# Optimization experiments

Hardware: AMD Instinct MI355X
Metric: run time of the kernel (lower is better)

The kernel has to match this reference:

```python
import jax, jax.numpy as jnp
import numpy as np

B, W, L = 64, 128, 32   # sentences, words per sentence, max chars per word
V, E, H = 128, 128, 256 # char vocab, char_embedding_size, word_embedding_size


def setup_inputs() -> dict:
    key = jax.random.key(0)
    ks = jax.random.split(key, 14)
    char_ids = jax.random.randint(ks[0], (B, W, L), 0, V, dtype=jnp.int32)
    word_lens = jax.random.randint(ks[1], (B, W), 1, L + 1, dtype=jnp.int32)
    sc = 1.0 / np.sqrt(H)
    n = lambda k, shape, s: (jax.random.normal(k, shape, jnp.float32) * s)
    emb_table = n(ks[2], (V, E), 1.0).at[0].set(0.0)  # padding_idx=0 row is zero
    return {
        "char_ids": char_ids,
        "word_lens": word_lens,
        "emb_table": emb_table,
        "Wih_f": n(ks[3], (4 * H, E), sc), "Whh_f": n(ks[4], (4 * H, H), sc),
        "bih_f": n(ks[5], (4 * H,), sc), "bhh_f": n(ks[6], (4 * H,), sc),
        "Wih_b": n(ks[7], (4 * H, E), sc), "Whh_b": n(ks[8], (4 * H, H), sc),
        "bih_b": n(ks[9], (4 * H,), sc), "bhh_b": n(ks[10], (4 * H,), sc),
        "pW": n(ks[11], (H, 2 * H), 1.0 / np.sqrt(2 * H)),
        "pb": n(ks[12], (H,), 1.0 / np.sqrt(2 * H)),
    }


def _lstm_dir(xW, mask, Whh, reverse):
    # xW: [N, L, 4H] precomputed x@Wih^T + biases; mask: [N, L] bool (t < len).
    # Masked scan: h/c freeze outside valid region, so the final carry is
    # h at t=len-1 (forward) or h at t=0 (backward, reverse=True).
    N = xW.shape[0]
    h0 = jnp.zeros((N, H), xW.dtype)
    c0 = jnp.zeros((N, H), xW.dtype)

    def step(carry, inp):
        h, c = carry
        xw_t, m_t = inp
        g = xw_t + h @ Whh.T                      # [N, 4H]
        i, f, gg, o = jnp.split(g, 4, axis=-1)    # PyTorch gate order i,f,g,o
        c_new = jax.nn.sigmoid(f) * c + jax.nn.sigmoid(i) * jnp.tanh(gg)
        h_new = jax.nn.sigmoid(o) * jnp.tanh(c_new)
        m = m_t[:, None]
        return (jnp.where(m, h_new, h), jnp.where(m, c_new, c)), None

    (h, _), _ = jax.lax.scan(step, (h0, c0),
                             (xW.transpose(1, 0, 2), mask.T), reverse=reverse)
    return h


def reference(char_ids, word_lens, emb_table, Wih_f, Whh_f, bih_f, bhh_f,
              Wih_b, Whh_b, bih_b, bhh_b, pW, pb):
    ids = char_ids.reshape(-1, L)                 # [N, L], N = B*W
    lens = word_lens.reshape(-1)                  # [N]
    x = emb_table[ids]                            # [N, L, E]
    mask = jnp.arange(L)[None, :] < lens[:, None] # [N, L]
    xWf = jnp.einsum('nle,ge->nlg', x, Wih_f) + (bih_f + bhh_f)
    xWb = jnp.einsum('nle,ge->nlg', x, Wih_b) + (bih_b + bhh_b)
    h_fwd = _lstm_dir(xWf, mask, Whh_f, reverse=False)  # fwd dir at last char
    h_bwd = _lstm_dir(xWb, mask, Whh_b, reverse=True)   # bwd dir at first char
    # Original concatenates (backward_at_first, forward_at_last)
    concat = jnp.concatenate([h_bwd, h_fwd], axis=-1)   # [N, 2H]
    wemb = concat @ pW.T + pb                           # [N, H]
    out = wemb.reshape(B, W, H)
    lens_out = jnp.full((B,), W, dtype=jnp.int32)       # words per sentence
    return out, lens_out
```

## Files before the change

### kernel.cpp

```cpp
#include <hip/hip_runtime.h>
#include <hip/hip_bf16.h>
#include <hip/hip_fp8.h>
#include <math.h>

#define B_  64
#define W_  128
#define L_  32
#define V_  128
#define E_  128
#define H_  256
#define G4_ 1024
#define NW  8192
#define KS_ 8
#define ROWB 264
#define HROW 264
#define M_  32

typedef long i64;
typedef short s8v  __attribute__((ext_vector_type(8)));
typedef float f4v  __attribute__((ext_vector_type(4)));

static __device__ __forceinline__ float b2f(unsigned short u) {
  return __uint_as_float(((unsigned int)u) << 16);
}
static __device__ __forceinline__ unsigned char f2fp8(float f) {
  __hip_fp8_e4m3 t(f);
  return (unsigned char)t.__x;
}
static __device__ __forceinline__ float sigm(float x) {
  return __builtin_amdgcn_rcpf(1.f + __expf(-x));
}
static __device__ __forceinline__ float tanh_(float x) {
  return __builtin_amdgcn_rcpf(1.f + __expf(-2.f * x)) * 2.f - 1.f;
}

__global__ __launch_bounds__(256) void k_embproj(
    const float* __restrict__ emb,
    const float* __restrict__ Wih_f, const float* __restrict__ bih_f, const float* __restrict__ bhh_f,
    const float* __restrict__ Wih_b, const float* __restrict__ bih_b, const float* __restrict__ bhh_b,
    unsigned short* __restrict__ ep4) {
  int v   = blockIdx.x & (V_ - 1);
  int dir = blockIdx.x >> 7;
  const float* Wih = dir ? Wih_b : Wih_f;
  const float* b1  = dir ? bih_b : bih_f;
  const float* b2  = dir ? bhh_b : bhh_f;
  __shared__ float es[E_];
  if (threadIdx.x < E_) es[threadIdx.x] = emb[v * E_ + threadIdx.x];
  __syncthreads();
#pragma unroll
  for (int q = 0; q < 4; ++q) {
    int g = q * 256 + threadIdx.x;
    const float* wr = Wih + g * E_;
    float a = 0.f;
#pragma unroll 4
    for (int k = 0; k < E_; k += 4) {
      float4 w4 = *(const float4*)(wr + k);
      float4 e4 = *(const float4*)(es + k);
      a += w4.x * e4.x + w4.y * e4.y + w4.z * e4.z + w4.w * e4.w;
    }
    int gate = g >> 8, col = g & 255;
    union { __hip_bfloat16 b; unsigned short u; } cv;
    cv.b = __float2bfloat16(a + b1[g] + b2[g]);
    ep4[((((dir * V_ + v) << 8) + col) << 2) + gate] = cv.u;
  }
}

__global__ __launch_bounds__(64) void k_pack(
    const float* __restrict__ Whh_f, const float* __restrict__ Whh_b,
    unsigned char* __restrict__ Bpack) {
  const int lane = threadIdx.x;
  const int f    = blockIdx.x & 7;
  const int w    = (blockIdx.x >> 3) & 7;
  const int ks   = (blockIdx.x >> 6) % KS_;
  const int dir  = blockIdx.x / (64 * KS_);
  const float* Whh = dir ? Whh_b : Whh_f;
  const int u  = f >> 1, jj = f & 1;
  const int nt = u * 16 + 2 * w + jj;
  const int n  = nt * 16 + (lane & 15);
  const int k0 = ks * 32 + (lane >> 4) * 8;
  size_t base = ((((size_t)(dir * KS_ + ks) * 8 + w) * 8 + f) * 64 + lane) * 8;
#pragma unroll
  for (int j = 0; j < 8; ++j)
    Bpack[base + j] = f2fp8(Whh[n * H_ + k0 + j]);
}

#define NCHUNK 32
#define CHSZ  (NW / NCHUNK)
__global__ __launch_bounds__(1024) void k_sort(const int* __restrict__ word_lens,
                                               int* __restrict__ perm) {
  __shared__ int cnt_s[NCHUNK][33];
  __shared__ int off_s[NCHUNK][33];
  const int tid = threadIdx.x;
  const int ch  = tid >> 5;
  const int ln  = (tid & 31) + 1;
  const int base = ch * CHSZ;
  int c = 0;
  for (int i = 0; i < CHSZ; ++i) c += (word_lens[base + i] == ln);
  cnt_s[ch][ln] = c;
  __syncthreads();
  if (tid == 0) {
    int run = 0;
    for (int l = 32; l >= 1; --l)
      for (int c2 = 0; c2 < NCHUNK; ++c2) { off_s[c2][l] = run; run += cnt_s[c2][l]; }
  }
  __syncthreads();
  int ptr = off_s[ch][ln];
  for (int i = 0; i < CHSZ; ++i) {
    int wi = base + i;
    if (word_lens[wi] == ln) perm[ptr++] = wi;
  }
}

__global__ __launch_bounds__(512, 4) void k_lstm(
    const int* __restrict__ char_ids, const int* __restrict__ word_lens,
    const int* __restrict__ perm, const unsigned short* __restrict__ ep4,
    const unsigned char* __restrict__ Bpack, unsigned short* __restrict__ hcat) {
  const int tid  = threadIdx.x;
  const int lane = tid & 63;
  const int w    = tid >> 6;
  const int bid  = blockIdx.x;
  const int q    = bid >> 7;
  const int dir  = q & 1;
  const int chunk = (bid < 256) ? (bid & 127) : ((q == 2) ? 511 - bid : 639 - bid);
  const int w0   = chunk * M_;

  __shared__ unsigned char  hL [M_][ROWB];
  __shared__ unsigned short hLb[M_][HROW];
  __shared__ int ids_s[M_][L_ + 1];
  __shared__ int len_s[M_];
  __shared__ int pw_s[M_];

  if (tid < M_) {
    int gw = perm[w0 + tid];
    pw_s[tid]  = gw;
    len_s[tid] = word_lens[gw];
  }
  __syncthreads();
  for (int i = tid; i < M_ * L_; i += 512) {
    int qq = i >> 5;
    ids_s[qq][i & 31] = char_ids[pw_s[qq] * L_ + (i & 31)];
  }
  for (int i = tid; i < M_ * ROWB / 4; i += 512) ((unsigned int*)hL)[i] = 0u;
  __syncthreads();

  const int mlen = len_s[0];
  unsigned lrp[2];
#pragma unroll
  for (int mt = 0; mt < 2; ++mt) {
    int bw = mt * 16 + ((lane >> 4) << 2);
    lrp[mt] = (unsigned)len_s[bw] | ((unsigned)len_s[bw + 1] << 8) |
              ((unsigned)len_s[bw + 2] << 16) | ((unsigned)len_s[bw + 3] << 24);
  }

  const char* Bb0 = (const char*)Bpack + (size_t)dir * (KS_ * 8 * 8 * 64 * 8)
                    + (size_t)w * (8 * 64 * 8) + (size_t)lane * 8;
  const char* ar = (const char*)&hL[lane & 15][0] + ((lane >> 4) << 3);
  const ushort4* epv = (const ushort4*)ep4 + ((size_t)dir << 15);
  const int p0 = 2 * w * 16 + (lane & 15);
  const int g4 = (lane >> 4) << 2;

  float c_[2][2][4];
#pragma unroll
  for (int jj = 0; jj < 2; ++jj)
#pragma unroll
    for (int mt = 0; mt < 2; ++mt)
#pragma unroll
      for (int r = 0; r < 4; ++r) c_[jj][mt][r] = 0.f;

  for (int t = 0; t < mlen; ++t) {
    f4v acc[4][2][2];
#pragma unroll
    for (int u = 0; u < 4; ++u)
#pragma unroll
      for (int jj = 0; jj < 2; ++jj)
#pragma unroll
        for (int mt = 0; mt < 2; ++mt) acc[u][jj][mt] = (f4v){0.f, 0.f, 0.f, 0.f};

    const char* bp0 = Bb0;
    const char* bp1 = Bb0 + 2048;
#pragma unroll 1
    for (int ks = 0; ks < KS_; ++ks) {
      i64 af0 = *(const i64*)(ar + ks * 32);
      i64 af1 = *(const i64*)(ar + 16 * ROWB + ks * 32);
      i64 b0 = *(const i64*)(bp0 + 0);
      i64 b1 = *(const i64*)(bp0 + 512);
      i64 b2 = *(const i64*)(bp0 + 1024);
      i64 b3 = *(const i64*)(bp0 + 1536);
      i64 b4 = *(const i64*)(bp1 + 0);
      i64 b5 = *(const i64*)(bp1 + 512);
      i64 b6 = *(const i64*)(bp1 + 1024);
      i64 b7 = *(const i64*)(bp1 + 1536);
      acc[0][0][0] = __builtin_amdgcn_mfma_f32_16x16x32_fp8_fp8(af0, b0, acc[0][0][0], 0, 0, 0);
      acc[0][0][1] = __builtin_amdgcn_mfma_f32_16x16x32_fp8_fp8(af1, b0, acc[0][0][1], 0, 0, 0);
      acc[0][1][0] = __builtin_amdgcn_mfma_f32_16x16x32_fp8_fp8(af0, b1, acc[0][1][0], 0, 0, 0);
      acc[0][1][1] = __builtin_amdgcn_mfma_f32_16x16x32_fp8_fp8(af1, b1, acc[0][1][1], 0, 0, 0);
      acc[1][0][0] = __builtin_amdgcn_mfma_f32_16x16x32_fp8_fp8(af0, b2, acc[1][0][0], 0, 0, 0);
      acc[1][0][1] = __builtin_amdgcn_mfma_f32_16x16x32_fp8_fp8(af1, b2, acc[1][0][1], 0, 0, 0);
      acc[1][1][0] = __builtin_amdgcn_mfma_f32_16x16x32_fp8_fp8(af0, b3, acc[1][1][0], 0, 0, 0);
      acc[1][1][1] = __builtin_amdgcn_mfma_f32_16x16x32_fp8_fp8(af1, b3, acc[1][1][1], 0, 0, 0);
      acc[2][0][0] = __builtin_amdgcn_mfma_f32_16x16x32_fp8_fp8(af0, b4, acc[2][0][0], 0, 0, 0);
      acc[2][0][1] = __builtin_amdgcn_mfma_f32_16x16x32_fp8_fp8(af1, b4, acc[2][0][1], 0, 0, 0);
      acc[2][1][0] = __builtin_amdgcn_mfma_f32_16x16x32_fp8_fp8(af0, b5, acc[2][1][0], 0, 0, 0);
      acc[2][1][1] = __builtin_amdgcn_mfma_f32_16x16x32_fp8_fp8(af1, b5, acc[2][1][1], 0, 0, 0);
      acc[3][0][0] = __builtin_amdgcn_mfma_f32_16x16x32_fp8_fp8(af0, b6, acc[3][0][0], 0, 0, 0);
      acc[3][0][1] = __builtin_amdgcn_mfma_f32_16x16x32_fp8_fp8(af1, b6, acc[3][0][1], 0, 0, 0);
      acc[3][1][0] = __builtin_amdgcn_mfma_f32_16x16x32_fp8_fp8(af0, b7, acc[3][1][0], 0, 0, 0);
      acc[3][1][1] = __builtin_amdgcn_mfma_f32_16x16x32_fp8_fp8(af1, b7, acc[3][1][1], 0, 0, 0);
      bp0 += 32768;
      bp1 += 32768;
    }

    __syncthreads();

#pragma unroll
    for (int mt = 0; mt < 2; ++mt) {
      ushort4 xc0[4], xc1[4];
      int act = 0, fin = 0;
#pragma unroll
      for (int r = 0; r < 4; ++r) {
        int len = (int)((lrp[mt] >> (8 * r)) & 255u);
        int tt  = dir ? max(len - 1 - t, 0) : t;
        int id  = ids_s[mt * 16 + g4 + r][tt];
        xc0[r] = epv[(id << 8) + p0];
        xc1[r] = epv[(id << 8) + p0 + 16];
        act |= (t < len)      ? (1 << r) : 0;
        fin |= (t == len - 1) ? (1 << r) : 0;
      }
#pragma unroll
      for (int jj = 0; jj < 2; ++jj) {
#pragma unroll
        for (int r = 0; r < 4; ++r) {
          ushort4 xw = jj ? xc1[r] : xc0[r];
          float gi = acc[0][jj][mt][r] + b2f(xw.x);
          float gf = acc[1][jj][mt][r] + b2f(xw.y);
          float gg = acc[2][jj][mt][r] + b2f(xw.z);
          float go = acc[3][jj][mt][r] + b2f(xw.w);
          float cn = sigm(gf) * c_[jj][mt][r] + sigm(gi) * tanh_(gg);
          float hn = sigm(go) * tanh_(cn);
          const int m = mt * 16 + g4 + r;
          const int p = (2 * w + jj) * 16 + (lane & 15);
          if ((act >> r) & 1) {
            c_[jj][mt][r] = cn;
            hL[m][p] = f2fp8(hn);
          }
          if ((fin >> r) & 1) {
            union { __hip_bfloat16 b; unsigned short u; } cv;
            cv.b = __float2bfloat16(hn);
            hLb[m][p] = cv.u;
          }
        }
      }
    }
    __syncthreads();
  }

  const int off = dir ? 0 : H_;
  for (int i = tid; i < M_ * H_ / 8; i += 512) {
    int qq  = i >> 5;
    int pos = (i & 31) << 3;
    s8v v = *(const s8v*)&hLb[qq][pos];
    *(s8v*)&hcat[(size_t)pw_s[qq] * (2 * H_) + off + pos] = v;
  }
}

#define PM_ 16
__global__ __launch_bounds__(256) void k_proj(
    const unsigned short* __restrict__ hcat, const float* __restrict__ pW,
    const float* __restrict__ pb, float* __restrict__ out) {
  const int tid = threadIdx.x;
  const int n0  = blockIdx.x * PM_;
  __shared__ float hs[PM_][2 * H_];
  for (int i = tid; i < PM_ * 2 * H_ / 8; i += 256) {
    s8v v = *(const s8v*)&hcat[(size_t)n0 * 2 * H_ + i * 8];
    float* d = (float*)hs + i * 8;
#pragma unroll
    for (int j = 0; j < 8; ++j) d[j] = b2f((unsigned short)v[j]);
  }
  __syncthreads();

  const float* pwr = pW + tid * (2 * H_);
  float acc[PM_];
#pragma unroll
  for (int m = 0; m < PM_; ++m) acc[m] = 0.f;

#pragma unroll 2
  for (int k = 0; k < 2 * H_; k += 4) {
    float4 w4 = *(const float4*)(pwr + k);
#pragma unroll
    for (int m = 0; m < PM_; ++m) {
      float4 h4 = *(const float4*)(&hs[m][k]);
      acc[m] += w4.x * h4.x + w4.y * h4.y + w4.z * h4.z + w4.w * h4.w;
    }
  }
  const float bias = pb[tid];
#pragma unroll
  for (int m = 0; m < PM_; ++m) out[(n0 + m) * H_ + tid] = acc[m] + bias;

  if (blockIdx.x == 0 && tid < B_) out[NW * H_ + tid] = (float)W_;
}

extern "C" void kernel_launch(void* const* d_in, const int* in_sizes, int n_in,
                              void* d_out, int out_size, void* d_ws, size_t ws_size,
                              hipStream_t stream) {
  const int*   char_ids  = (const int*)  d_in[0];
  const int*   word_lens = (const int*)  d_in[1];
  const float* emb       = (const float*)d_in[2];
  const float* Wih_f     = (const float*)d_in[3];
  const float* Whh_f     = (const float*)d_in[4];
  const float* bih_f     = (const float*)d_in[5];
  const float* bhh_f     = (const float*)d_in[6];
  const float* Wih_b     = (const float*)d_in[7];
  const float* Whh_b     = (const float*)d_in[8];
  const float* bih_b     = (const float*)d_in[9];
  const float* bhh_b     = (const float*)d_in[10];
  const float* pW        = (const float*)d_in[11];
  const float* pb        = (const float*)d_in[12];
  float* out = (float*)d_out;

  const size_t BPACK_BYTES = (size_t)2 * KS_ * 8 * 8 * 64 * 8;
  const size_t EP4_BYTES   = (size_t)2 * V_ * 256 * 4 * 2;
  unsigned char* Bpack = (unsigned char*)d_ws;
  unsigned short* ep4 = (unsigned short*)((char*)d_ws + BPACK_BYTES);
  int* perm = (int*)((char*)d_ws + BPACK_BYTES + EP4_BYTES);
  unsigned short* hcat = (unsigned short*)((char*)d_ws + BPACK_BYTES + EP4_BYTES + NW * sizeof(int));

  k_sort<<<dim3(1), dim3(1024), 0, stream>>>(word_lens, perm);
  k_embproj<<<dim3(2 * V_), dim3(256), 0, stream>>>(emb, Wih_f, bih_f, bhh_f,
                                                    Wih_b, bih_b, bhh_b, ep4);
  k_pack<<<dim3(2 * KS_ * 64), dim3(64), 0, stream>>>(Whh_f, Whh_b, Bpack);
  k_lstm<<<dim3(512), dim3(512), 0, stream>>>(char_ids, word_lens, perm, ep4, Bpack, hcat);
  k_proj<<<dim3(NW / PM_), dim3(256), 0, stream>>>(hcat, pW, pb, out);
}
```

Before: 399.4 us.

## Double-buffer LSTM hidden state in LDS and merge prep kernels into one launch

```diff
diff --git a/kernel.cpp b/kernel.cpp
--- a/kernel.cpp
+++ b/kernel.cpp
@@ -34,23 +34,29 @@
   return __builtin_amdgcn_rcpf(1.f + __expf(-2.f * x)) * 2.f - 1.f;
 }
 
-__global__ __launch_bounds__(256) void k_embproj(
+#define NCHUNK 32
+#define CHSZ  (NW / NCHUNK)
+__global__ __launch_bounds__(1024) void k_prep(
+    const int* __restrict__ word_lens,
     const float* __restrict__ emb,
     const float* __restrict__ Wih_f, const float* __restrict__ bih_f, const float* __restrict__ bhh_f,
     const float* __restrict__ Wih_b, const float* __restrict__ bih_b, const float* __restrict__ bhh_b,
-    unsigned short* __restrict__ ep4) {
-  int v   = blockIdx.x & (V_ - 1);
-  int dir = blockIdx.x >> 7;
-  const float* Wih = dir ? Wih_b : Wih_f;
-  const float* b1  = dir ? bih_b : bih_f;
-  const float* b2  = dir ? bhh_b : bhh_f;
-  __shared__ float es[E_];
-  if (threadIdx.x < E_) es[threadIdx.x] = emb[v * E_ + threadIdx.x];
-  __syncthreads();
-#pragma unroll
-  for (int q = 0; q < 4; ++q) {
-    int g = q * 256 + threadIdx.x;
-    const float* wr = Wih + g * E_;
+    const float* __restrict__ Whh_f, const float* __restrict__ Whh_b,
+    unsigned short* __restrict__ ep4, int* __restrict__ perm,
+    unsigned char* __restrict__ Bpack) {
+  const int bb  = blockIdx.x;
+  const int tid = threadIdx.x;
+
+  if (bb < 256) {
+    int v   = bb & (V_ - 1);
+    int dir = bb >> 7;
+    const float* Wih = dir ? Wih_b : Wih_f;
+    const float* b1  = dir ? bih_b : bih_f;
+    const float* b2  = dir ? bhh_b : bhh_f;
+    __shared__ float es[E_];
+    if (tid < E_) es[tid] = emb[v * E_ + tid];
+    __syncthreads();
+    const float* wr = Wih + tid * E_;
     float a = 0.f;
 #pragma unroll 4
     for (int k = 0; k < E_; k += 4) {
@@ -58,56 +64,47 @@
       float4 e4 = *(const float4*)(es + k);
       a += w4.x * e4.x + w4.y * e4.y + w4.z * e4.z + w4.w * e4.w;
     }
-    int gate = g >> 8, col = g & 255;
+    int gate = tid >> 8, col = tid & 255;
     union { __hip_bfloat16 b; unsigned short u; } cv;
-    cv.b = __float2bfloat16(a + b1[g] + b2[g]);
+    cv.b = __float2bfloat16(a + b1[tid] + b2[tid]);
     ep4[((((dir * V_ + v) << 8) + col) << 2) + gate] = cv.u;
-  }
-}
-
-__global__ __launch_bounds__(64) void k_pack(
-    const float* __restrict__ Whh_f, const float* __restrict__ Whh_b,
-    unsigned char* __restrict__ Bpack) {
-  const int lane = threadIdx.x;
-  const int f    = blockIdx.x & 7;
-  const int w    = (blockIdx.x >> 3) & 7;
-  const int ks   = (blockIdx.x >> 6) % KS_;
-  const int dir  = blockIdx.x / (64 * KS_);
-  const float* Whh = dir ? Whh_b : Whh_f;
-  const int u  = f >> 1, jj = f & 1;
-  const int nt = u * 16 + 2 * w + jj;
-  const int n  = nt * 16 + (lane & 15);
-  const int k0 = ks * 32 + (lane >> 4) * 8;
-  size_t base = ((((size_t)(dir * KS_ + ks) * 8 + w) * 8 + f) * 64 + lane) * 8;
-#pragma unroll
-  for (int j = 0; j < 8; ++j)
-    Bpack[base + j] = f2fp8(Whh[n * H_ + k0 + j]);
-}
-
-#define NCHUNK 32
-#define CHSZ  (NW / NCHUNK)
-__global__ __launch_bounds__(1024) void k_sort(const int* __restrict__ word_lens,
-                                               int* __restrict__ perm) {
-  __shared__ int cnt_s[NCHUNK][33];
-  __shared__ int off_s[NCHUNK][33];
-  const int tid = threadIdx.x;
-  const int ch  = tid >> 5;
-  const int ln  = (tid & 31) + 1;
-  const int base = ch * CHSZ;
-  int c = 0;
-  for (int i = 0; i < CHSZ; ++i) c += (word_lens[base + i] == ln);
-  cnt_s[ch][ln] = c;
-  __syncthreads();
-  if (tid == 0) {
-    int run = 0;
-    for (int l = 32; l >= 1; --l)
-      for (int c2 = 0; c2 < NCHUNK; ++c2) { off_s[c2][l] = run; run += cnt_s[c2][l]; }
-  }
-  __syncthreads();
-  int ptr = off_s[ch][ln];
-  for (int i = 0; i < CHSZ; ++i) {
-    int wi = base + i;
-    if (word_lens[wi] == ln) perm[ptr++] = wi;
+  } else if (bb == 256) {
+    __shared__ int cnt_s[NCHUNK][33];
+    __shared__ int off_s[NCHUNK][33];
+    const int ch  = tid >> 5;
+    const int ln  = (tid & 31) + 1;
+    const int base = ch * CHSZ;
+    int c = 0;
+    for (int i = 0; i < CHSZ; ++i) c += (word_lens[base + i] == ln);
+    cnt_s[ch][ln] = c;
+    __syncthreads();
+    if (tid == 0) {
+      int run = 0;
+      for (int l = 32; l >= 1; --l)
+        for (int c2 = 0; c2 < NCHUNK; ++c2) { off_s[c2][l] = run; run += cnt_s[c2][l]; }
+    }
+    __syncthreads();
+    int ptr = off_s[ch][ln];
+    for (int i = 0; i < CHSZ; ++i) {
+      int wi = base + i;
+      if (word_lens[wi] == ln) perm[ptr++] = wi;
+    }
+  } else {
+    int tile = (bb - 257) * 16 + (tid >> 6);
+    const int lane = tid & 63;
+    const int f    = tile & 7;
+    const int w    = (tile >> 3) & 7;
+    const int ks   = (tile >> 6) % KS_;
+    const int dir  = tile / (64 * KS_);
+    const float* Whh = dir ? Whh_b : Whh_f;
+    const int u  = f >> 1, jj = f & 1;
+    const int nt = u * 16 + 2 * w + jj;
+    const int n  = nt * 16 + (lane & 15);
+    const int k0 = ks * 32 + (lane >> 4) * 8;
+    size_t base = ((((size_t)(dir * KS_ + ks) * 8 + w) * 8 + f) * 64 + lane) * 8;
+#pragma unroll
+    for (int j = 0; j < 8; ++j)
+      Bpack[base + j] = f2fp8(Whh[n * H_ + k0 + j]);
   }
 }
 
@@ -124,7 +121,7 @@
   const int chunk = (bid < 256) ? (bid & 127) : ((q == 2) ? 511 - bid : 639 - bid);
   const int w0   = chunk * M_;
 
-  __shared__ unsigned char  hL [M_][ROWB];
+  __shared__ unsigned char  hL[2][M_][ROWB];
   __shared__ unsigned short hLb[M_][HROW];
   __shared__ int ids_s[M_][L_ + 1];
   __shared__ int len_s[M_];
@@ -140,7 +137,7 @@
     int qq = i >> 5;
     ids_s[qq][i & 31] = char_ids[pw_s[qq] * L_ + (i & 31)];
   }
-  for (int i = tid; i < M_ * ROWB / 4; i += 512) ((unsigned int*)hL)[i] = 0u;
+  for (int i = tid; i < M_ * ROWB / 4; i += 512) ((unsigned int*)hL[0])[i] = 0u;
   __syncthreads();
 
   const int mlen = len_s[0];
@@ -154,7 +151,10 @@
 
   const char* Bb0 = (const char*)Bpack + (size_t)dir * (KS_ * 8 * 8 * 64 * 8)
                     + (size_t)w * (8 * 64 * 8) + (size_t)lane * 8;
-  const char* ar = (const char*)&hL[lane & 15][0] + ((lane >> 4) << 3);
+  const char* arA = (const char*)&hL[0][lane & 15][0] + ((lane >> 4) << 3);
+  const char* arB = arA + M_ * ROWB;
+  unsigned char* hwA = &hL[0][0][0];
+  unsigned char* hwB = &hL[1][0][0];
   const ushort4* epv = (const ushort4*)ep4 + ((size_t)dir << 15);
   const int p0 = 2 * w * 16 + (lane & 15);
   const int g4 = (lane >> 4) << 2;
@@ -168,6 +168,7 @@
       for (int r = 0; r < 4; ++r) c_[jj][mt][r] = 0.f;
 
   for (int t = 0; t < mlen; ++t) {
+    const char* ar = (t & 1) ? arB : arA;
     f4v acc[4][2][2];
 #pragma unroll
     for (int u = 0; u < 4; ++u)
@@ -210,8 +211,7 @@
       bp1 += 32768;
     }
 
-    __syncthreads();
-
+    unsigned char* hwb = (t & 1) ? hwA : hwB;
 #pragma unroll
     for (int mt = 0; mt < 2; ++mt) {
       ushort4 xc0[4], xc1[4];
@@ -241,7 +241,7 @@
           const int p = (2 * w + jj) * 16 + (lane & 15);
           if ((act >> r) & 1) {
             c_[jj][mt][r] = cn;
-            hL[m][p] = f2fp8(hn);
+            hwb[m * ROWB + p] = f2fp8(hn);
           }
           if ((fin >> r) & 1) {
             union { __hip_bfloat16 b; unsigned short u; } cv;
@@ -324,10 +324,10 @@
   int* perm = (int*)((char*)d_ws + BPACK_BYTES + EP4_BYTES);
   unsigned short* hcat = (unsigned short*)((char*)d_ws + BPACK_BYTES + EP4_BYTES + NW * sizeof(int));
 
-  k_sort<<<dim3(1), dim3(1024), 0, stream>>>(word_lens, perm);
-  k_embproj<<<dim3(2 * V_), dim3(256), 0, stream>>>(emb, Wih_f, bih_f, bhh_f,
-                                                    Wih_b, bih_b, bhh_b, ep4);
-  k_pack<<<dim3(2 * KS_ * 64), dim3(64), 0, stream>>>(Whh_f, Whh_b, Bpack);
+  k_prep<<<dim3(321), dim3(1024), 0, stream>>>(word_lens, emb,
+                                               Wih_f, bih_f, bhh_f,
+                                               Wih_b, bih_b, bhh_b,
+                                               Whh_f, Whh_b, ep4, perm, Bpack);
   k_lstm<<<dim3(512), dim3(512), 0, stream>>>(char_ids, word_lens, perm, ep4, Bpack, hcat);
   k_proj<<<dim3(NW / PM_), dim3(256), 0, stream>>>(hcat, pW, pb, out);
 }
```

Result: faster. 390.7 us (-2.2%).
